# Kernel tuning notes

Measured on AMD Instinct MI355X. Metric: run time of the kernel, lower is better.

## Reference

```python
import jax, jax.numpy as jnp
import numpy as np

D_MODEL = 512
D_HEAD = 64
N_HEADS = D_MODEL // D_HEAD  # 8
KSIZE = 7


def setup_inputs() -> dict:
    key = jax.random.key(0)
    k1, k2, k3 = jax.random.split(key, 3)
    x = jax.random.normal(k1, (2, 48, 48, D_MODEL), dtype=jnp.float32)
    # torch Linear(d, 3d, bias=False): y = x @ W.T ; store transposed weight directly
    w_qkv = jax.random.normal(k2, (D_MODEL, 3 * D_MODEL), dtype=jnp.float32) * 0.02
    w_out = jax.random.normal(k3, (D_MODEL, D_MODEL), dtype=jnp.float32) * 0.02
    return {"x": x, "w_qkv": w_qkv, "w_out": w_out}


def _nbhd_idx(L, k):
    # NATTEN semantics: window centered at each pixel, shifted (clamped) to stay
    # fully inside the image near borders. Returns [L, k] absolute indices.
    start = jnp.clip(jnp.arange(L) - k // 2, 0, L - k)
    return start[:, None] + jnp.arange(k)[None, :]


def reference(x, w_qkv, w_out):
    n, h, w, _ = x.shape
    qkv = (x @ w_qkv).reshape(n, h, w, 3, N_HEADS, D_HEAD)
    qkv = jnp.transpose(qkv, (3, 0, 4, 1, 2, 5))  # [3, n, nh, h, w, e]
    q, k, v = qkv[0], qkv[1], qkv[2]
    q = q / jnp.asarray(D_HEAD, q.dtype) ** 0.5

    ih = _nbhd_idx(h, KSIZE)  # [h, k]
    iw = _nbhd_idx(w, KSIZE)  # [w, k]
    IH = ih[:, None, :, None]  # [h,1,k,1]
    IW = iw[None, :, None, :]  # [1,w,1,k]

    # gather per-pixel 2D neighborhoods: [n, nh, h, w, ka, kb, e]
    k_nb = k[:, :, IH, IW, :]
    logits = jnp.einsum('nghwe,nghwabe->nghwab', q, k_nb)
    logits = logits.reshape(n, N_HEADS, h, w, KSIZE * KSIZE)
    attn = jax.nn.softmax(logits, axis=-1).reshape(n, N_HEADS, h, w, KSIZE, KSIZE)

    v_nb = v[:, :, IH, IW, :]
    o = jnp.einsum('nghwab,nghwabe->nghwe', attn, v_nb)  # [n, nh, h, w, e]
    o = jnp.transpose(o, (0, 2, 3, 1, 4)).reshape(n, h, w, N_HEADS * D_HEAD)
    return o @ w_out
```

## Files before the change

kernel.cpp:

```cpp
#include <hip/hip_runtime.h>
#include <hip/hip_bf16.h>

typedef __bf16 bf16x4 __attribute__((ext_vector_type(4)));
typedef __bf16 bf16x8 __attribute__((ext_vector_type(8)));
typedef float f32x4 __attribute__((ext_vector_type(4)));

#define N_PIX 4608
#define D_MODEL 512
#define QKV_N 1536

__device__ __forceinline__ void gload_lds16(const void* g, void* l) {
  __builtin_amdgcn_global_load_lds(
      (const __attribute__((address_space(1))) unsigned int*)g,
      (__attribute__((address_space(3))) unsigned int*)l, 16, 0, 0);
}

__global__ __launch_bounds__(256) void prep_kernel(
    const float* __restrict__ x, const float* __restrict__ wq,
    const float* __restrict__ wo, __bf16* __restrict__ xbf,
    __bf16* __restrict__ wqT, __bf16* __restrict__ woT) {
  int b = blockIdx.x, tid = threadIdx.x;
  if (b < 2304) {
    int i = b * 1024 + tid * 4;
    float4 v = *(const float4*)&x[i];
    bf16x4 o = {(__bf16)v.x, (__bf16)v.y, (__bf16)v.z, (__bf16)v.w};
    *(bf16x4*)&xbf[i] = o;
    return;
  }
  __shared__ float tile[32][33];
  const float* src; __bf16* dst; int R, C, bx, by;
  bool is_wq;
  if (b < 3072) {
    int t = b - 2304; src = wq; dst = wqT; R = 512; C = 1536;
    bx = (t % 48) * 32; by = (t / 48) * 32; is_wq = true;
  } else {
    int t = b - 3072; src = wo; dst = woT; R = 512; C = 512;
    bx = (t & 15) * 32; by = (t >> 4) * 32; is_wq = false;
  }
  int tx = tid & 31, ty = tid >> 5;
#pragma unroll
  for (int i = 0; i < 32; i += 8)
    tile[ty + i][tx] = src[(by + ty + i) * C + bx + tx];
  __syncthreads();
#pragma unroll
  for (int i = 0; i < 32; i += 8) {
    int outrow = bx + ty + i;
    float v = tile[tx][ty + i];
    if (is_wq && outrow < 512) v *= 0.125f;
    dst[outrow * R + by + tx] = (__bf16)v;
  }
}

template <int BM, int BN>
__global__ __launch_bounds__(256) void gemm_kernel(
    const __bf16* __restrict__ A, const __bf16* __restrict__ Bt,
    void* __restrict__ C, int M, int N, int K, int c_is_f32) {
  constexpr int MT = BM / 32;
  constexpr int NT = BN / 32;
  constexpr int AR = BM / 4;
  constexpr int BR = BN / 4;
  __shared__ __bf16 sA[2][BM * 32];
  __shared__ __bf16 sB[2][BN * 32];
  int tid = threadIdx.x;
  int wv = tid >> 6, lane = tid & 63;
  int quad = lane >> 4, r16 = lane & 15;
  int m0 = blockIdx.y * BM, n0 = blockIdx.x * BN;

  int rA = lane >> 2;
  int kc = (lane & 3) * 8;
  const __bf16* Ag0 = A + (long)(m0 + wv * AR + rA) * K + kc;
  const __bf16* Bg0 = Bt + (long)(n0 + wv * BR + rA) * K + kc;

  int mw = (wv & 1) * (BM / 2), nw = (wv >> 1) * (BN / 2);

  f32x4 acc[MT][NT];
#pragma unroll
  for (int mt = 0; mt < MT; ++mt)
#pragma unroll
    for (int nt = 0; nt < NT; ++nt) acc[mt][nt] = f32x4{0.f, 0.f, 0.f, 0.f};

  auto stage = [&](int buf, int k0) {
    gload_lds16(Ag0 + k0, &sA[buf][(wv * AR) * 32]);
    if (AR == 32)
      gload_lds16(Ag0 + (long)16 * K + k0, &sA[buf][(wv * AR + 16) * 32]);
    gload_lds16(Bg0 + k0, &sB[buf][(wv * BR) * 32]);
    if (BR == 32)
      gload_lds16(Bg0 + (long)16 * K + k0, &sB[buf][(wv * BR + 16) * 32]);
  };

  stage(0, 0);
  int cur = 0;
  for (int k0 = 0; k0 < K; k0 += 32) {
    __syncthreads();
    if (k0 + 32 < K) stage(cur ^ 1, k0 + 32);
    bf16x8 af[MT], bfr[NT];
#pragma unroll
    for (int mt = 0; mt < MT; ++mt)
      af[mt] = *(const bf16x8*)&sA[cur][(mw + mt * 16 + r16) * 32 + quad * 8];
#pragma unroll
    for (int nt = 0; nt < NT; ++nt)
      bfr[nt] = *(const bf16x8*)&sB[cur][(nw + nt * 16 + r16) * 32 + quad * 8];
#pragma unroll
    for (int mt = 0; mt < MT; ++mt)
#pragma unroll
      for (int nt = 0; nt < NT; ++nt)
        acc[mt][nt] = __builtin_amdgcn_mfma_f32_16x16x32_bf16(af[mt], bfr[nt], acc[mt][nt], 0, 0, 0);
    cur ^= 1;
  }

  __bf16* Cb = (__bf16*)C;
  float* Cf = (float*)C;
#pragma unroll
  for (int mt = 0; mt < MT; ++mt)
#pragma unroll
    for (int r = 0; r < 4; ++r) {
      int row = m0 + mw + mt * 16 + quad * 4 + r;
#pragma unroll
      for (int nt = 0; nt < NT; ++nt) {
        int col = n0 + nw + nt * 16 + r16;
        float v = acc[mt][nt][r];
        if (c_is_f32) Cf[(long)row * N + col] = v;
        else          Cb[(long)row * N + col] = (__bf16)v;
      }
    }
}

#define KSTR 72
__global__ __launch_bounds__(512) void natten_attn_kernel(
    const __bf16* __restrict__ qkv, __bf16* __restrict__ o) {
  __shared__ __bf16 sK[196 * KSTR];
  __shared__ __bf16 sV[196 * KSTR];
  int tid = threadIdx.x;
  int bid = blockIdx.x;
  int nB = bid / 288;
  int rem = bid - nB * 288;
  int head = rem / 36;
  int tile = rem - head * 36;
  int tr = tile / 6, tc = tile - tr * 6;
  int r0 = tr * 8, c0 = tc * 8;
  int loH = r0 - 3; loH = loH < 0 ? 0 : (loH > 41 ? 41 : loH);
  int loW = c0 - 3; loW = loW < 0 ? 0 : (loW > 41 ? 41 : loW);

  for (int j = tid; j < 196 * 8; j += 512) {
    int rowi = j >> 3, ch = j & 7;
    int rr = rowi / 14, cc = rowi - rr * 14;
    int hh = loH + rr; hh = hh > 47 ? 47 : hh;
    int wp = loW + cc; wp = wp > 47 ? 47 : wp;
    long base = (long)(nB * 2304 + hh * 48 + wp) * QKV_N + head * 64 + ch * 8;
    *(uint4*)&sK[rowi * KSTR + ch * 8] = *(const uint4*)&qkv[base + 512];
    *(uint4*)&sV[rowi * KSTR + ch * 8] = *(const uint4*)&qkv[base + 1024];
  }
  __syncthreads();

  int q = tid >> 3, s = tid & 7;
  int qr = q >> 3, qc = q & 7;
  int h = r0 + qr, w = c0 + qc;
  int pix = nB * 2304 + h * 48 + w;
  int hs = h - 3; hs = hs < 0 ? 0 : (hs > 41 ? 41 : hs); hs -= loH;
  int ws = w - 3; ws = ws < 0 ? 0 : (ws > 41 ? 41 : ws); ws -= loW;
  int base = (hs * 14 + ws) * KSTR + s * 8;

  bf16x8 q0 = *(const bf16x8*)&qkv[(long)pix * QKV_N + head * 64 + s * 8];
  float qf[8];
#pragma unroll
  for (int t = 0; t < 8; ++t) qf[t] = (float)q0[t];

  float lg[49];
#pragma unroll
  for (int j = 0; j < 49; ++j) {
    int a = j / 7, b = j % 7;
    bf16x8 k0 = *(const bf16x8*)&sK[base + (a * 14 + b) * KSTR];
    float acc = 0.f;
#pragma unroll
    for (int t = 0; t < 8; ++t) acc = fmaf(qf[t], (float)k0[t], acc);
    acc += __shfl_xor(acc, 1);
    acc += __shfl_xor(acc, 2);
    acc += __shfl_xor(acc, 4);
    lg[j] = acc;
  }

  float mx = lg[0];
#pragma unroll
  for (int j = 1; j < 49; ++j) mx = fmaxf(mx, lg[j]);
  float sm = 0.f;
#pragma unroll
  for (int j = 0; j < 49; ++j) { lg[j] = __expf(lg[j] - mx); sm += lg[j]; }
  float inv = 1.f / sm;

  float ov[8];
#pragma unroll
  for (int t = 0; t < 8; ++t) ov[t] = 0.f;
#pragma unroll
  for (int j = 0; j < 49; ++j) {
    int a = j / 7, b = j % 7;
    float pj = lg[j] * inv;
    bf16x8 v0 = *(const bf16x8*)&sV[base + (a * 14 + b) * KSTR];
#pragma unroll
    for (int t = 0; t < 8; ++t) ov[t] = fmaf(pj, (float)v0[t], ov[t]);
  }

  bf16x8 o0;
#pragma unroll
  for (int t = 0; t < 8; ++t) o0[t] = (__bf16)ov[t];
  *(bf16x8*)&o[(long)pix * D_MODEL + head * 64 + s * 8] = o0;
}


extern "C" void kernel_launch(void* const* d_in, const int* in_sizes, int n_in,
                              void* d_out, int out_size, void* d_ws, size_t ws_size,
                              hipStream_t stream) {
  const float* x = (const float*)d_in[0];
  const float* w_qkv = (const float*)d_in[1];
  const float* w_out = (const float*)d_in[2];
  float* out = (float*)d_out;

  __bf16* ws = (__bf16*)d_ws;
  __bf16* xbf   = ws;
  __bf16* wqkvT = xbf + N_PIX * D_MODEL;
  __bf16* woutT = wqkvT + QKV_N * D_MODEL;
  __bf16* qkvb  = woutT + D_MODEL * D_MODEL;
  __bf16* obf   = qkvb + N_PIX * QKV_N;

  prep_kernel<<<3328, 256, 0, stream>>>(x, w_qkv, w_out, xbf, wqkvT, woutT);
  gemm_kernel<64, 128><<<dim3(QKV_N / 128, N_PIX / 64), 256, 0, stream>>>(
      xbf, wqkvT, qkvb, N_PIX, QKV_N, D_MODEL, 0);
  natten_attn_kernel<<<576, 512, 0, stream>>>(qkvb, obf);
  gemm_kernel<64, 64><<<dim3(D_MODEL / 64, N_PIX / 64), 256, 0, stream>>>(
      obf, woutT, out, N_PIX, D_MODEL, D_MODEL, 1);
}
```

Before: 121.7 us.

## Double GEMM K-tile to 64 and use bf16 dot2 for attention logits

The GEMM kernel now stages 64-wide K slices per iteration instead of 32. Each lane loads 8 rows with 16-byte global-to-LDS copies, and the kernel runs two MFMA sub-steps per barrier, halving the number of syncs and loop iterations. This doubles LDS use per block and may cost occupancy or introduce bank conflicts with the 128-byte row stride. In the attention kernel, the q·k dot product uses the fdot2 bf16 instruction when available, replacing eight scalar converts and FMAs, with slightly different rounding.

```diff
diff --git a/kernel.cpp b/kernel.cpp
--- a/kernel.cpp
+++ b/kernel.cpp
@@ -1,6 +1,7 @@
 #include <hip/hip_runtime.h>
 #include <hip/hip_bf16.h>
 
+typedef __bf16 bf16x2 __attribute__((ext_vector_type(2)));
 typedef __bf16 bf16x4 __attribute__((ext_vector_type(4)));
 typedef __bf16 bf16x8 __attribute__((ext_vector_type(8)));
 typedef float f32x4 __attribute__((ext_vector_type(4)));
@@ -59,17 +60,17 @@
   constexpr int NT = BN / 32;
   constexpr int AR = BM / 4;
   constexpr int BR = BN / 4;
-  __shared__ __bf16 sA[2][BM * 32];
-  __shared__ __bf16 sB[2][BN * 32];
+  __shared__ __bf16 sA[2][BM * 64];
+  __shared__ __bf16 sB[2][BN * 64];
   int tid = threadIdx.x;
   int wv = tid >> 6, lane = tid & 63;
   int quad = lane >> 4, r16 = lane & 15;
   int m0 = blockIdx.y * BM, n0 = blockIdx.x * BN;
 
-  int rA = lane >> 2;
-  int kc = (lane & 3) * 8;
-  const __bf16* Ag0 = A + (long)(m0 + wv * AR + rA) * K + kc;
-  const __bf16* Bg0 = Bt + (long)(n0 + wv * BR + rA) * K + kc;
+  int rr = lane >> 3;
+  int kc = (lane & 7) * 8;
+  const __bf16* Ag = A + (long)(m0 + wv * AR + rr) * K + kc;
+  const __bf16* Bg = Bt + (long)(n0 + wv * BR + rr) * K + kc;
 
   int mw = (wv & 1) * (BM / 2), nw = (wv >> 1) * (BN / 2);
 
@@ -80,31 +81,34 @@
     for (int nt = 0; nt < NT; ++nt) acc[mt][nt] = f32x4{0.f, 0.f, 0.f, 0.f};
 
   auto stage = [&](int buf, int k0) {
-    gload_lds16(Ag0 + k0, &sA[buf][(wv * AR) * 32]);
-    if (AR == 32)
-      gload_lds16(Ag0 + (long)16 * K + k0, &sA[buf][(wv * AR + 16) * 32]);
-    gload_lds16(Bg0 + k0, &sB[buf][(wv * BR) * 32]);
-    if (BR == 32)
-      gload_lds16(Bg0 + (long)16 * K + k0, &sB[buf][(wv * BR + 16) * 32]);
+#pragma unroll
+    for (int g = 0; g < AR / 8; ++g)
+      gload_lds16(Ag + (long)(g * 8) * K + k0, &sA[buf][(wv * AR + g * 8) * 64]);
+#pragma unroll
+    for (int g = 0; g < BR / 8; ++g)
+      gload_lds16(Bg + (long)(g * 8) * K + k0, &sB[buf][(wv * BR + g * 8) * 64]);
   };
 
   stage(0, 0);
   int cur = 0;
-  for (int k0 = 0; k0 < K; k0 += 32) {
+  for (int k0 = 0; k0 < K; k0 += 64) {
     __syncthreads();
-    if (k0 + 32 < K) stage(cur ^ 1, k0 + 32);
-    bf16x8 af[MT], bfr[NT];
-#pragma unroll
-    for (int mt = 0; mt < MT; ++mt)
-      af[mt] = *(const bf16x8*)&sA[cur][(mw + mt * 16 + r16) * 32 + quad * 8];
-#pragma unroll
-    for (int nt = 0; nt < NT; ++nt)
-      bfr[nt] = *(const bf16x8*)&sB[cur][(nw + nt * 16 + r16) * 32 + quad * 8];
-#pragma unroll
-    for (int mt = 0; mt < MT; ++mt)
+    if (k0 + 64 < K) stage(cur ^ 1, k0 + 64);
+#pragma unroll
+    for (int s = 0; s < 2; ++s) {
+      bf16x8 af[MT], bfr[NT];
+#pragma unroll
+      for (int mt = 0; mt < MT; ++mt)
+        af[mt] = *(const bf16x8*)&sA[cur][(mw + mt * 16 + r16) * 64 + s * 32 + quad * 8];
 #pragma unroll
       for (int nt = 0; nt < NT; ++nt)
-        acc[mt][nt] = __builtin_amdgcn_mfma_f32_16x16x32_bf16(af[mt], bfr[nt], acc[mt][nt], 0, 0, 0);
+        bfr[nt] = *(const bf16x8*)&sB[cur][(nw + nt * 16 + r16) * 64 + s * 32 + quad * 8];
+#pragma unroll
+      for (int mt = 0; mt < MT; ++mt)
+#pragma unroll
+        for (int nt = 0; nt < NT; ++nt)
+          acc[mt][nt] = __builtin_amdgcn_mfma_f32_16x16x32_bf16(af[mt], bfr[nt], acc[mt][nt], 0, 0, 0);
+    }
     cur ^= 1;
   }
 
@@ -143,8 +147,8 @@
 
   for (int j = tid; j < 196 * 8; j += 512) {
     int rowi = j >> 3, ch = j & 7;
-    int rr = rowi / 14, cc = rowi - rr * 14;
-    int hh = loH + rr; hh = hh > 47 ? 47 : hh;
+    int rrh = rowi / 14, cc = rowi - rrh * 14;
+    int hh = loH + rrh; hh = hh > 47 ? 47 : hh;
     int wp = loW + cc; wp = wp > 47 ? 47 : wp;
     long base = (long)(nB * 2304 + hh * 48 + wp) * QKV_N + head * 64 + ch * 8;
     *(uint4*)&sK[rowi * KSTR + ch * 8] = *(const uint4*)&qkv[base + 512];
@@ -171,8 +175,17 @@
     int a = j / 7, b = j % 7;
     bf16x8 k0 = *(const bf16x8*)&sK[base + (a * 14 + b) * KSTR];
     float acc = 0.f;
+#if __has_builtin(__builtin_amdgcn_fdot2_f32_bf16)
+#pragma unroll
+    for (int t = 0; t < 4; ++t) {
+      bf16x2 qa = {q0[2 * t], q0[2 * t + 1]};
+      bf16x2 ka = {k0[2 * t], k0[2 * t + 1]};
+      acc = __builtin_amdgcn_fdot2_f32_bf16(qa, ka, acc, false);
+    }
+#else
 #pragma unroll
     for (int t = 0; t < 8; ++t) acc = fmaf(qf[t], (float)k0[t], acc);
+#endif
     acc += __shfl_xor(acc, 1);
     acc += __shfl_xor(acc, 2);
     acc += __shfl_xor(acc, 4);
```

Result: slower. 125.8 us (+3.4%).
